# Optimization experiments

Measured on AMD Instinct MI355X. Metric: run time of the kernel, lower is better.

The kernel has to match this reference:

```python
import jax, jax.numpy as jnp
import numpy as np

B, H, W, C = 16, 128, 128, 64
S = 2  # unpool size (2, 2)


def setup_inputs() -> dict:
    key = jax.random.key(0)
    k1, k2, k3 = jax.random.split(key, 3)
    updates = jax.random.normal(k1, (B, H, W, C), dtype=jnp.float32)
    Ho, Wo = H * S, W * S
    # Build valid max_pool_with_argmax-style mask: each pooled element maps to a
    # random cell inside its own SxS window in the output, flat index over (Ho,Wo,C).
    dy = jax.random.randint(k2, (B, H, W, C), 0, S)
    dx = jax.random.randint(k3, (B, H, W, C), 0, S)
    h = jnp.arange(H)[:, None, None]   # (H,1,1)
    w = jnp.arange(W)[:, None]         # (W,1)
    c = jnp.arange(C)                  # (C,)
    mask = ((S * h + dy) * Wo + (S * w + dx)) * C + c
    return {"updates": updates, "mask": mask.astype(jnp.int32)}


def reference(updates, mask):
    b_, h_, w_, c_ = updates.shape
    Ho, Wo = h_ * S, w_ * S
    m = mask.astype(jnp.int32)
    # Decode flat per-batch index (over Ho*Wo*C) into (y, x); feature index is the
    # channel position itself, batch index is the batch position (as in the original).
    y = m // (Wo * C)
    x = (m // C) % Wo
    bidx = jnp.broadcast_to(jnp.arange(b_, dtype=jnp.int32)[:, None, None, None], m.shape)
    fidx = jnp.broadcast_to(jnp.arange(c_, dtype=jnp.int32), m.shape)
    # tf.scatter_nd sums duplicate indices -> .at[].add matches exactly.
    out = jnp.zeros((b_, Ho, Wo, c_), dtype=updates.dtype).at[bidx, y, x, fidx].add(updates)
    return out
```

## Files before the change

kernel.cpp:

```cpp
#include <hip/hip_runtime.h>


typedef float f32x4 __attribute__((ext_vector_type(4)));
typedef int   i32x4 __attribute__((ext_vector_type(4)));

__global__ __launch_bounds__(256) void MaxUnpooling2D_13589276524630_kernel(
        const f32x4* __restrict__ upd,
        const i32x4* __restrict__ msk,
        f32x4*       __restrict__ out)
{
    const int t0 = blockIdx.x * (4 * 256) + threadIdx.x;

    f32x4 u[4];
    i32x4 m[4];
#pragma unroll
    for (int j = 0; j < 4; ++j) {
        u[j] = __builtin_nontemporal_load(&upd[t0 + j * 256]);
        m[j] = __builtin_nontemporal_load(&msk[t0 + j * 256]);
    }

#pragma unroll
    for (int j = 0; j < 4; ++j) {
        const int tid = t0 + j * 256;
        const int c = (tid & 15) << 2;
        const int w = (tid >> 4) & 127;
        const int h = (tid >> 11) & 127;
        const int b = tid >> 18;

        const int obase_b = b << 22;
        const int y0 = 2 * h;
        const int x0 = 2 * w;

        int   fb[4];
        f32x4 v[4];
#pragma unroll
        for (int py = 0; py < 2; ++py) {
#pragma unroll
            for (int px = 0; px < 2; ++px) {
                const int i = py * 2 + px;
                fb[i] = (((y0 + py) << 8) + (x0 + px)) * 64 + c;
                v[i].x = (m[j].x == fb[i]    ) ? u[j].x : 0.0f;
                v[i].y = (m[j].y == fb[i] + 1) ? u[j].y : 0.0f;
                v[i].z = (m[j].z == fb[i] + 2) ? u[j].z : 0.0f;
                v[i].w = (m[j].w == fb[i] + 3) ? u[j].w : 0.0f;
            }
        }
#pragma unroll
        for (int i = 0; i < 4; ++i)
            __builtin_nontemporal_store(v[i], &out[(obase_b + fb[i]) >> 2]);
    }
}

extern "C" void kernel_launch(void* const* d_in, const int* in_sizes, int n_in,
                              void* d_out, int out_size, void* d_ws, size_t ws_size,
                              hipStream_t stream) {
    const f32x4* upd = (const f32x4*)d_in[0];
    const i32x4* msk = (const i32x4*)d_in[1];
    f32x4*       out = (f32x4*)d_out;

    const int n_groups = 16 * 128 * 128 * (64 / 4);
    const int block = 256;
    const int grid = n_groups / (block * 4);

    MaxUnpooling2D_13589276524630_kernel<<<grid, block, 0, stream>>>(upd, msk, out);
}
```

Before: 343.2 us.

## Remap threads over output columns so stores are contiguous, reloading inputs twice

Each thread now covers one output column x and writes two rows (y=2h and 2h+1) instead of covering a pooled cell and writing a 2x2 window. Adjacent lanes therefore write contiguous output addresses, which makes the store stream fully coalesced. The cost is that each input element is read by two threads. The kernel also drops nontemporal loads so the second read can hit in cache, and it doubles the grid size.

```diff
diff --git a/kernel.cpp b/kernel.cpp
--- a/kernel.cpp
+++ b/kernel.cpp
@@ -9,45 +9,45 @@
         const i32x4* __restrict__ msk,
         f32x4*       __restrict__ out)
 {
-    const int t0 = blockIdx.x * (4 * 256) + threadIdx.x;
+    const int p0 = blockIdx.x * (4 * 256) + threadIdx.x;
 
     f32x4 u[4];
     i32x4 m[4];
 #pragma unroll
     for (int j = 0; j < 4; ++j) {
-        u[j] = __builtin_nontemporal_load(&upd[t0 + j * 256]);
-        m[j] = __builtin_nontemporal_load(&msk[t0 + j * 256]);
+        const int p  = p0 + j * 256;
+        const int c4 = p & 15;
+        const int x  = (p >> 4) & 255;
+        const int bh = p >> 12;
+        const int in_g = (bh << 11) | ((x >> 1) << 4) | c4;
+        u[j] = upd[in_g];
+        m[j] = msk[in_g];
     }
 
 #pragma unroll
     for (int j = 0; j < 4; ++j) {
-        const int tid = t0 + j * 256;
-        const int c = (tid & 15) << 2;
-        const int w = (tid >> 4) & 127;
-        const int h = (tid >> 11) & 127;
-        const int b = tid >> 18;
+        const int p  = p0 + j * 256;
+        const int c4 = p & 15;
+        const int x  = (p >> 4) & 255;
+        const int h  = (p >> 12) & 127;
+        const int b  = p >> 19;
 
-        const int obase_b = b << 22;
-        const int y0 = 2 * h;
-        const int x0 = 2 * w;
+        const int fb0 = (((h << 9) | x) << 6) | (c4 << 2);
+        const int fb1 = fb0 + 256 * 64;
 
-        int   fb[4];
-        f32x4 v[4];
-#pragma unroll
-        for (int py = 0; py < 2; ++py) {
-#pragma unroll
-            for (int px = 0; px < 2; ++px) {
-                const int i = py * 2 + px;
-                fb[i] = (((y0 + py) << 8) + (x0 + px)) * 64 + c;
-                v[i].x = (m[j].x == fb[i]    ) ? u[j].x : 0.0f;
-                v[i].y = (m[j].y == fb[i] + 1) ? u[j].y : 0.0f;
-                v[i].z = (m[j].z == fb[i] + 2) ? u[j].z : 0.0f;
-                v[i].w = (m[j].w == fb[i] + 3) ? u[j].w : 0.0f;
-            }
-        }
-#pragma unroll
-        for (int i = 0; i < 4; ++i)
-            __builtin_nontemporal_store(v[i], &out[(obase_b + fb[i]) >> 2]);
+        f32x4 v0, v1;
+        v0.x = (m[j].x == fb0    ) ? u[j].x : 0.0f;
+        v0.y = (m[j].y == fb0 + 1) ? u[j].y : 0.0f;
+        v0.z = (m[j].z == fb0 + 2) ? u[j].z : 0.0f;
+        v0.w = (m[j].w == fb0 + 3) ? u[j].w : 0.0f;
+        v1.x = (m[j].x == fb1    ) ? u[j].x : 0.0f;
+        v1.y = (m[j].y == fb1 + 1) ? u[j].y : 0.0f;
+        v1.z = (m[j].z == fb1 + 2) ? u[j].z : 0.0f;
+        v1.w = (m[j].w == fb1 + 3) ? u[j].w : 0.0f;
+
+        const int og0 = ((b << 22) + fb0) >> 2;
+        __builtin_nontemporal_store(v0, &out[og0]);
+        __builtin_nontemporal_store(v1, &out[og0 + (256 * 64 / 4)]);
     }
 }
 
@@ -58,9 +58,9 @@
     const i32x4* msk = (const i32x4*)d_in[1];
     f32x4*       out = (f32x4*)d_out;
 
-    const int n_groups = 16 * 128 * 128 * (64 / 4);
+    const int n_pairs = 16 * 128 * 256 * 16;
     const int block = 256;
-    const int grid = n_groups / (block * 4);
+    const int grid = n_pairs / (block * 4);
 
     MaxUnpooling2D_13589276524630_kernel<<<grid, block, 0, stream>>>(upd, msk, out);
 }
```

Result: slower. 352.4 us (+2.7%).
